# Performance work log

Measured on AMD Instinct MI355X. Metric: run time of the kernel, lower is better.

The kernel has to match this reference:

```python
import jax, jax.numpy as jnp
import numpy as np

NEG_SLOPE = 0.2  # LeakyReLU slope used by GAT attention
EPS = 1e-16


def segment_softmax(scores, seg, num_segments):
    # numerically-stable softmax over edges grouped by destination node
    m = jax.ops.segment_max(scores, seg, num_segments=num_segments)
    ex = jnp.exp(scores - m[seg])
    s = jax.ops.segment_sum(ex, seg, num_segments=num_segments)
    return ex / (s[seg] + EPS)


def gat_conv(x, edge_index, W, a_src, a_dst, b):
    # x: [N, d_in], edge_index: [2, E], W: [d_in, d_out], a_*: [d_out], b: [d_out]
    n = x.shape[0]
    h = x @ W                                   # [N, d_out]
    src, dst = edge_index[0], edge_index[1]     # [E], [E]
    alpha_src = h @ a_src                       # [N]
    alpha_dst = h @ a_dst                       # [N]
    e = jax.nn.leaky_relu(alpha_src[src] + alpha_dst[dst], NEG_SLOPE)  # [E]
    alpha = segment_softmax(e, dst, n)          # [E]
    out = jax.ops.segment_sum(h[src] * alpha[:, None], dst, num_segments=n)  # [N, d_out]
    return out + b


def setup_inputs() -> dict:
    key = jax.random.key(0)
    ks = jax.random.split(key, 12)
    N, D, E = 100000, 64, 1600000
    x = jax.random.normal(ks[0], (N, D), dtype=jnp.float32)
    edge_index = jax.random.randint(ks[1], (2, E), 0, N, dtype=jnp.int64)
    s = 1.0 / np.sqrt(D)
    W1 = jax.random.normal(ks[2], (D, D), dtype=jnp.float32) * s
    a_src1 = jax.random.normal(ks[3], (D,), dtype=jnp.float32) * s
    a_dst1 = jax.random.normal(ks[4], (D,), dtype=jnp.float32) * s
    b1 = jnp.zeros((D,), dtype=jnp.float32)
    W2 = jax.random.normal(ks[5], (D, D), dtype=jnp.float32) * s
    a_src2 = jax.random.normal(ks[6], (D,), dtype=jnp.float32) * s
    a_dst2 = jax.random.normal(ks[7], (D,), dtype=jnp.float32) * s
    b2 = jnp.zeros((D,), dtype=jnp.float32)
    return {"x": x, "edge_index": edge_index,
            "W1": W1, "a_src1": a_src1, "a_dst1": a_dst1, "b1": b1,
            "W2": W2, "a_src2": a_src2, "a_dst2": a_dst2, "b2": b2}


def reference(x, edge_index, W1, a_src1, a_dst1, b1, W2, a_src2, a_dst2, b2):
    # Encoder.forward: conv_near on first 500 edges, conv_include on the rest
    x = gat_conv(x, edge_index[:, :500], W1, a_src1, a_dst1, b1)
    return gat_conv(x, edge_index[:, 500:], W2, a_src2, a_dst2, b2)
```

## Files before the change

### kernel.cpp

```cpp
#include <hip/hip_runtime.h>


#define LRELU(v) ((v) >= 0.0f ? (v) : 0.2f * (v))
#define EPSF 1e-16f
#define NB 128
#define BCAP 512
#define BMW 3200

struct P {
    const float* x; const int* EI; int E, N;
    const float *W1, *a_src1, *a_dst1, *b1, *W2, *a_src2, *a_dst2, *b2;
    float* F;
    int* bcnt;
    int* idx_map;
    int* map2;
    float* s_spec;
    float* adsp;
    char* flag;
    unsigned* srcbm;
    unsigned* dstbm;
    float* as2tab; float* ad2tab; float* h2tab;
    int* slw; int* nxt;
    float4* out;
};

__device__ __forceinline__ float wred_sum(float v) {
    for (int o = 32; o; o >>= 1) v += __shfl_xor(v, o);
    return v;
}
__device__ __forceinline__ int wred_min(int v) {
    for (int o = 32; o; o >>= 1) v = min(v, __shfl_xor(v, o));
    return v;
}
__device__ __forceinline__ bool bittest(const unsigned* bm, int n) {
    return (bm[n >> 5] >> (n & 31)) & 1u;
}

__global__ __launch_bounds__(256) void initk(P p) {
    int i = blockIdx.x * 256 + threadIdx.x;
    if (i < p.N) { p.map2[i] = -1; p.s_spec[i] = 0.f; p.flag[i] = 0; }
    if (i < BMW) { p.srcbm[i] = 0u; p.dstbm[i] = 0u; }
    if (i < NB * 16) p.bcnt[i] = 0;
    if (blockIdx.x == 0 && threadIdx.x < 64) {
        int t = threadIdx.x;
        float hb = 0.f;
        for (int k = 0; k < 64; ++k) hb += p.b1[k] * p.W2[k * 64 + t];
        p.F[128 + t] = hb;
        float as = wred_sum(hb * p.a_src2[t]);
        float ad = wred_sum(hb * p.a_dst2[t]);
        if (t == 0) { p.F[192] = as; p.F[193] = ad; }
    }
}

__global__ __launch_bounds__(256) void l1k(P p) {
    const int w = (blockIdx.x * 256 + threadIdx.x) >> 6;
    const int lane = threadIdx.x & 63;
    if (w >= 500) return;

    const float4* W1r = (const float4*)(p.W1 + lane * 64);
    const float4* as1 = (const float4*)p.a_src1;
    const float4* ad1 = (const float4*)p.a_dst1;
    float wsl = 0.f, wdl = 0.f;
    #pragma unroll
    for (int l = 0; l < 16; ++l) {
        float4 wv = W1r[l], av = as1[l], bv = ad1[l];
        wsl += wv.x * av.x + wv.y * av.y + wv.z * av.z + wv.w * av.w;
        wdl += wv.x * bv.x + wv.y * bv.y + wv.z * bv.z + wv.w * bv.w;
    }
    const float hbl = p.F[128 + lane];

    const int d = p.EI[p.E + w];
    int firstj = 1 << 30;
    for (int r = 0; r < 8; ++r) {
        int j = r * 64 + lane;
        if (j < 500 && p.EI[p.E + j] == d) firstj = min(firstj, j);
    }
    firstj = wred_min(firstj);
    if (firstj != w) return;
    if (lane == 0) {
        p.idx_map[d] = w;
        atomicOr(&p.srcbm[d >> 5], 1u << (d & 31));
    }

    const float dv = wred_sum(p.x[(long)d * 64 + lane] * wdl);
    float Ssum = 0.f, e1w = 0.f, x1l = 0.f;
    bool fm = true;
    for (int r = 0; r < 8; ++r) {
        int j = r * 64 + lane;
        bool m = (j < 500) && (p.EI[p.E + j] == d);
        unsigned long long mask = __ballot(m);
        while (mask) {
            int j0 = r * 64 + (int)__ffsll(mask) - 1;
            mask &= mask - 1;
            int sj = p.EI[j0];
            float xs = p.x[(long)sj * 64 + lane];
            float e1j = LRELU(wred_sum(xs * wsl) + dv);
            float ew;
            if (fm) { e1w = e1j; ew = 1.f; fm = false; }
            else ew = expf(e1j - e1w);
            Ssum += ew;
            float h1l = 0.f;
            #pragma unroll
            for (int k = 0; k < 64; ++k) h1l = fmaf(__shfl(xs, k), p.W1[k * 64 + lane], h1l);
            x1l = fmaf(ew, h1l, x1l);
        }
    }
    float x1 = x1l / (Ssum + EPSF) + p.b1[lane];
    float h2l = 0.f;
    #pragma unroll
    for (int k = 0; k < 64; ++k) h2l = fmaf(__shfl(x1, k), p.W2[k * 64 + lane], h2l);
    p.h2tab[w * 64 + lane] = h2l - hbl;
    float as = wred_sum(h2l * p.a_src2[lane]);
    float ad = wred_sum(h2l * p.a_dst2[lane]);
    if (lane == 0) { p.as2tab[w] = as; p.ad2tab[w] = ad; }
}

__device__ __forceinline__ void specEdge(const P& p, long e, int s, int bkt,
                                         float asb, float adb) {
    if (!bittest(p.srcbm, s)) return;
    int sl = p.idx_map[s];
    int d = p.EI[p.E + e];
    float ad2v = bittest(p.srcbm, d) ? p.ad2tab[p.idx_map[d]] : adb;
    float md  = LRELU(asb + ad2v);
    float esp = LRELU(p.as2tab[sl] + ad2v);
    atomicAdd(&p.s_spec[d], expf(esp - md) - 1.0f);
    p.adsp[d] = ad2v;
    atomicOr(&p.dstbm[d >> 5], 1u << (d & 31));
    int i = atomicAdd(&p.bcnt[bkt * 16], 1);
    if (i < BCAP) {
        int pos = bkt * BCAP + i;
        p.slw[pos] = sl;
        p.nxt[pos] = atomicExch(&p.map2[d], pos);
    }
}

__global__ __launch_bounds__(256) void scanAk(P p) {
    long q = (long)blockIdx.x * 256 + threadIdx.x;
    long base = 500 + q * 4;
    if (base >= p.E) return;
    const float asb = p.F[192], adb = p.F[193];
    int bkt = (int)(q & (NB - 1));
    if (base + 3 < p.E) {
        int4 s4 = *(const int4*)(p.EI + base);
        specEdge(p, base + 0, s4.x, bkt, asb, adb);
        specEdge(p, base + 1, s4.y, bkt, asb, adb);
        specEdge(p, base + 2, s4.z, bkt, asb, adb);
        specEdge(p, base + 3, s4.w, bkt, asb, adb);
    } else {
        for (long e = base; e < p.E; ++e) specEdge(p, e, p.EI[e], bkt, asb, adb);
    }
}

__device__ __forceinline__ void dstEdge(const P& p, int d) {
    p.flag[d] = 1;
    if (bittest(p.dstbm, d)) atomicAdd(&p.s_spec[d], 1.0f);
}

__global__ __launch_bounds__(256) void scanBk(P p) {
    long q = (long)blockIdx.x * 256 + threadIdx.x;
    long base = 500 + q * 4;
    if (base >= p.E) return;
    if (base + 3 < p.E) {
        int4 d4 = *(const int4*)(p.EI + p.E + base);
        dstEdge(p, d4.x); dstEdge(p, d4.y); dstEdge(p, d4.z); dstEdge(p, d4.w);
    } else {
        for (long e = base; e < p.E; ++e) dstEdge(p, p.EI[p.E + e]);
    }
}

__global__ __launch_bounds__(256) void outk(P p) {
    long t = (long)blockIdx.x * 256 + threadIdx.x;
    if (t >= (long)p.N * 16) return;
    int n = (int)(t >> 4), qq = (int)(t & 15);
    float coef = p.flag[n] ? 1.0f : 0.0f;
    float4 hb4 = ((const float4*)(p.F + 128))[qq];
    float4 b24 = ((const float4*)p.b2)[qq];
    float4 o;
    o.x = b24.x + coef * hb4.x; o.y = b24.y + coef * hb4.y;
    o.z = b24.z + coef * hb4.z; o.w = b24.w + coef * hb4.w;
    if (bittest(p.dstbm, n)) {
        float den = p.s_spec[n] + EPSF;
        float ad2v = p.adsp[n];
        float md = LRELU(p.F[192] + ad2v);
        int pos = p.map2[n];
        while (pos >= 0) {
            int sl = p.slw[pos];
            float w = expf(LRELU(p.as2tab[sl] + ad2v) - md) / den;
            float4 h4 = ((const float4*)(p.h2tab + sl * 64))[qq];
            o.x = fmaf(w, h4.x, o.x); o.y = fmaf(w, h4.y, o.y);
            o.z = fmaf(w, h4.z, o.z); o.w = fmaf(w, h4.w, o.w);
            pos = p.nxt[pos];
        }
    }
    p.out[t] = o;
}

extern "C" void kernel_launch(void* const* d_in, const int* in_sizes, int n_in,
                              void* d_out, int out_size, void* d_ws, size_t ws_size,
                              hipStream_t stream) {
    P p;
    p.x      = (const float*)d_in[0];
    p.EI     = (const int*)d_in[1];
    p.W1     = (const float*)d_in[2];
    p.a_src1 = (const float*)d_in[3];
    p.a_dst1 = (const float*)d_in[4];
    p.b1     = (const float*)d_in[5];
    p.W2     = (const float*)d_in[6];
    p.a_src2 = (const float*)d_in[7];
    p.a_dst2 = (const float*)d_in[8];
    p.b2     = (const float*)d_in[9];
    p.out    = (float4*)d_out;
    p.N = in_sizes[0] / 64;
    p.E = in_sizes[1] / 2;

    char* base = (char*)d_ws;
    p.F       = (float*)base;
    p.bcnt    = (int*)(base + 1024);
    p.idx_map = p.bcnt + NB * 16;
    p.map2    = p.idx_map + p.N;
    p.s_spec  = (float*)(p.map2 + p.N);
    p.adsp    = p.s_spec + p.N;
    p.flag    = (char*)(p.adsp + p.N);
    char* q   = p.flag + p.N;
    q = (char*)(((uintptr_t)q + 63) & ~(uintptr_t)63);
    p.srcbm   = (unsigned*)q;
    p.dstbm   = p.srcbm + BMW;
    p.as2tab  = (float*)(p.dstbm + BMW);
    p.ad2tab  = p.as2tab + 512;
    p.h2tab   = p.ad2tab + 512;
    p.slw     = (int*)(p.h2tab + 512 * 64);
    p.nxt     = p.slw + NB * BCAP;

    long quads = ((long)p.E - 500 + 3) / 4;
    int scanBlocks = (int)((quads + 255) / 256);

    initk <<<(p.N + 255) / 256, 256, 0, stream>>>(p);
    l1k   <<<125, 256, 0, stream>>>(p);
    scanAk<<<scanBlocks, 256, 0, stream>>>(p);
    scanBk<<<scanBlocks, 256, 0, stream>>>(p);
    outk  <<<(int)(((long)p.N * 16 + 255) / 256), 256, 0, stream>>>(p);
}
```

Measured before the change: 59.21 us.

## Move per-node init and bias precompute into l1k, shrink initk, grid-stride outk

Moves the per-node initialization of map2, s_spec and flag out of initk into the l1k kernel, and l1k now launches enough blocks to cover all N nodes. The b1·W2 bias vector is recomputed per lane inside l1k rather than read from F, with warp 0 writing F and the attention scalars. initk shrinks to clearing only the bitmaps and bucket counters. scanAk and scanBk drop their tail-handling branch and always do an int4 load; outk becomes a grid-stride loop over a fixed 2560 blocks. The aim is to cut one large launch and some branching. Each of the 500 l1k warps now repeats a 64-step loop to compute the bias vector. Dropping the tail path relies on E-500 being a multiple of 4; otherwise the last int4 load reads past the end of the edge array.

```diff
diff --git a/kernel.cpp b/kernel.cpp
--- a/kernel.cpp
+++ b/kernel.cpp
@@ -38,23 +38,16 @@
 
 __global__ __launch_bounds__(256) void initk(P p) {
     int i = blockIdx.x * 256 + threadIdx.x;
-    if (i < p.N) { p.map2[i] = -1; p.s_spec[i] = 0.f; p.flag[i] = 0; }
     if (i < BMW) { p.srcbm[i] = 0u; p.dstbm[i] = 0u; }
     if (i < NB * 16) p.bcnt[i] = 0;
-    if (blockIdx.x == 0 && threadIdx.x < 64) {
-        int t = threadIdx.x;
-        float hb = 0.f;
-        for (int k = 0; k < 64; ++k) hb += p.b1[k] * p.W2[k * 64 + t];
-        p.F[128 + t] = hb;
-        float as = wred_sum(hb * p.a_src2[t]);
-        float ad = wred_sum(hb * p.a_dst2[t]);
-        if (t == 0) { p.F[192] = as; p.F[193] = ad; }
-    }
 }
 
 __global__ __launch_bounds__(256) void l1k(P p) {
-    const int w = (blockIdx.x * 256 + threadIdx.x) >> 6;
-    const int lane = threadIdx.x & 63;
+    const int tid = blockIdx.x * 256 + threadIdx.x;
+    const int nth = gridDim.x * 256;
+    for (int i = tid; i < p.N; i += nth) { p.map2[i] = -1; p.s_spec[i] = 0.f; p.flag[i] = 0; }
+
+    const int w = tid >> 6, lane = threadIdx.x & 63;
     if (w >= 500) return;
 
     const float4* W1r = (const float4*)(p.W1 + lane * 64);
@@ -67,7 +60,15 @@
         wsl += wv.x * av.x + wv.y * av.y + wv.z * av.z + wv.w * av.w;
         wdl += wv.x * bv.x + wv.y * bv.y + wv.z * bv.z + wv.w * bv.w;
     }
-    const float hbl = p.F[128 + lane];
+    float hbl = 0.f;
+    for (int k = 0; k < 64; ++k) hbl = fmaf(p.b1[k], p.W2[k * 64 + lane], hbl);
+
+    if (w == 0) {
+        p.F[128 + lane] = hbl;
+        float asb = wred_sum(hbl * p.a_src2[lane]);
+        float adb = wred_sum(hbl * p.a_dst2[lane]);
+        if (lane == 0) { p.F[192] = asb; p.F[193] = adb; }
+    }
 
     const int d = p.EI[p.E + w];
     int firstj = 1 << 30;
@@ -140,15 +141,11 @@
     if (base >= p.E) return;
     const float asb = p.F[192], adb = p.F[193];
     int bkt = (int)(q & (NB - 1));
-    if (base + 3 < p.E) {
-        int4 s4 = *(const int4*)(p.EI + base);
-        specEdge(p, base + 0, s4.x, bkt, asb, adb);
-        specEdge(p, base + 1, s4.y, bkt, asb, adb);
-        specEdge(p, base + 2, s4.z, bkt, asb, adb);
-        specEdge(p, base + 3, s4.w, bkt, asb, adb);
-    } else {
-        for (long e = base; e < p.E; ++e) specEdge(p, e, p.EI[e], bkt, asb, adb);
-    }
+    int4 s4 = *(const int4*)(p.EI + base);
+    specEdge(p, base + 0, s4.x, bkt, asb, adb);
+    specEdge(p, base + 1, s4.y, bkt, asb, adb);
+    specEdge(p, base + 2, s4.z, bkt, asb, adb);
+    specEdge(p, base + 3, s4.w, bkt, asb, adb);
 }
 
 __device__ __forceinline__ void dstEdge(const P& p, int d) {
@@ -160,39 +157,37 @@
     long q = (long)blockIdx.x * 256 + threadIdx.x;
     long base = 500 + q * 4;
     if (base >= p.E) return;
-    if (base + 3 < p.E) {
-        int4 d4 = *(const int4*)(p.EI + p.E + base);
-        dstEdge(p, d4.x); dstEdge(p, d4.y); dstEdge(p, d4.z); dstEdge(p, d4.w);
-    } else {
-        for (long e = base; e < p.E; ++e) dstEdge(p, p.EI[p.E + e]);
-    }
+    int4 d4 = *(const int4*)(p.EI + p.E + base);
+    dstEdge(p, d4.x); dstEdge(p, d4.y); dstEdge(p, d4.z); dstEdge(p, d4.w);
 }
 
 __global__ __launch_bounds__(256) void outk(P p) {
-    long t = (long)blockIdx.x * 256 + threadIdx.x;
-    if (t >= (long)p.N * 16) return;
-    int n = (int)(t >> 4), qq = (int)(t & 15);
-    float coef = p.flag[n] ? 1.0f : 0.0f;
-    float4 hb4 = ((const float4*)(p.F + 128))[qq];
-    float4 b24 = ((const float4*)p.b2)[qq];
-    float4 o;
-    o.x = b24.x + coef * hb4.x; o.y = b24.y + coef * hb4.y;
-    o.z = b24.z + coef * hb4.z; o.w = b24.w + coef * hb4.w;
-    if (bittest(p.dstbm, n)) {
-        float den = p.s_spec[n] + EPSF;
-        float ad2v = p.adsp[n];
-        float md = LRELU(p.F[192] + ad2v);
-        int pos = p.map2[n];
-        while (pos >= 0) {
-            int sl = p.slw[pos];
-            float w = expf(LRELU(p.as2tab[sl] + ad2v) - md) / den;
-            float4 h4 = ((const float4*)(p.h2tab + sl * 64))[qq];
-            o.x = fmaf(w, h4.x, o.x); o.y = fmaf(w, h4.y, o.y);
-            o.z = fmaf(w, h4.z, o.z); o.w = fmaf(w, h4.w, o.w);
-            pos = p.nxt[pos];
+    const long M = (long)p.N * 16;
+    const long nth = (long)gridDim.x * 256;
+    for (long t = (long)blockIdx.x * 256 + threadIdx.x; t < M; t += nth) {
+        int n = (int)(t >> 4), qq = (int)(t & 15);
+        float coef = p.flag[n] ? 1.0f : 0.0f;
+        float4 hb4 = ((const float4*)(p.F + 128))[qq];
+        float4 b24 = ((const float4*)p.b2)[qq];
+        float4 o;
+        o.x = b24.x + coef * hb4.x; o.y = b24.y + coef * hb4.y;
+        o.z = b24.z + coef * hb4.z; o.w = b24.w + coef * hb4.w;
+        if (bittest(p.dstbm, n)) {
+            float den = p.s_spec[n] + EPSF;
+            float ad2v = p.adsp[n];
+            float md = LRELU(p.F[192] + ad2v);
+            int pos = p.map2[n];
+            while (pos >= 0) {
+                int sl = p.slw[pos];
+                float w = expf(LRELU(p.as2tab[sl] + ad2v) - md) / den;
+                float4 h4 = ((const float4*)(p.h2tab + sl * 64))[qq];
+                o.x = fmaf(w, h4.x, o.x); o.y = fmaf(w, h4.y, o.y);
+                o.z = fmaf(w, h4.z, o.z); o.w = fmaf(w, h4.w, o.w);
+                pos = p.nxt[pos];
+            }
         }
-    }
-    p.out[t] = o;
+        p.out[t] = o;
+    }
 }
 
 extern "C" void kernel_launch(void* const* d_in, const int* in_sizes, int n_in,
@@ -233,10 +228,11 @@
 
     long quads = ((long)p.E - 500 + 3) / 4;
     int scanBlocks = (int)((quads + 255) / 256);
-
-    initk <<<(p.N + 255) / 256, 256, 0, stream>>>(p);
-    l1k   <<<125, 256, 0, stream>>>(p);
+    int l1Blocks = (p.N + 255) / 256;
+
+    initk <<<(BMW + 255) / 256, 256, 0, stream>>>(p);
+    l1k   <<<l1Blocks, 256, 0, stream>>>(p);
     scanAk<<<scanBlocks, 256, 0, stream>>>(p);
     scanBk<<<scanBlocks, 256, 0, stream>>>(p);
-    outk  <<<(int)(((long)p.N * 16 + 255) / 256), 256, 0, stream>>>(p);
-}
+    outk  <<<2560, 256, 0, stream>>>(p);
+}
```

New measurement: 60.47 us. 2.1% more time.
